# Optimization experiments

Measured on AMD Instinct MI355X. Metric: run time of the kernel, lower is better.

## Reference

```python
import jax, jax.numpy as jnp
import numpy as np

BETA = 0.25
STRIDE = 64  # LCCombine: ConvTranspose1d with ones kernel, kernel_size == stride


def setup_inputs() -> dict:
    key = jax.random.key(0)
    k0, k1, k2, k3 = jax.random.split(key, 4)
    B, Q, K, N = 2, 64, 512, 1024
    n_classes = 256
    n_wav = N * STRIDE - 1
    quant_pred = jax.random.normal(k0, (B, n_classes, n_wav), dtype=jnp.float32)
    ze = jax.random.normal(k1, (B, Q, N), dtype=jnp.float32)
    emb = jax.random.normal(k2, (K, N), dtype=jnp.float32)
    target_wav = jax.random.randint(k3, (B, 1, n_wav), 0, n_classes)
    return {"quant_pred": quant_pred, "ze": ze, "emb": emb, "target_wav": target_wav}


def _combine(x):
    # LCCombine: replicate each bottleneck-rate value over STRIDE wav steps
    # (transposed conv, ones kernel, kernel==stride), then drop last step.
    # x: (B, N) -> (B, 1, N*STRIDE - 1)
    return jnp.repeat(x, STRIDE, axis=-1)[:, None, :-1]


def reference(quant_pred, ze, emb, target_wav):
    # l2 loss: stop-grad on ze (codebook update term)
    sg_ze = jax.lax.stop_gradient(ze)
    d = sg_ze[:, :, None, :] - emb[None, None, :, :]      # (B, Q, K, N)
    l2_loss = jnp.min(jnp.sum(d * d, axis=1), axis=1)      # (B, N)
    # commitment loss: stop-grad on emb
    sg_emb = jax.lax.stop_gradient(emb)
    dc = ze[:, :, None, :] - sg_emb[None, None, :, :]      # (B, Q, K, N)
    com_loss = jnp.min(jnp.sum(dc * dc, axis=1), axis=1) * BETA  # (B, N)

    l2_loss_comb = _combine(l2_loss)                       # (B, 1, N_wav)
    com_loss_comb = _combine(com_loss)                     # (B, 1, N_wav)

    log_pred = jax.nn.log_softmax(quant_pred, axis=1)      # (B, C, N_wav)
    log_pred_target = jnp.take_along_axis(log_pred, target_wav, axis=1)  # (B,1,N_wav)

    total_loss_terms = log_pred_target + l2_loss_comb + com_loss_comb
    return jnp.mean(total_loss_terms)
```

## Files before the change

### kernel.cpp

```cpp
#include <hip/hip_runtime.h>


#define QQ   64
#define NN   1024
#define KK   512
#define CLS  256
#define NW   65535

__global__ __launch_bounds__(64) void vq_l2min_kernel(
        const float* __restrict__ ze,
        const float* __restrict__ emb,
        float* __restrict__ l2ws,
        float* __restrict__ out) {
    int bn = blockIdx.x;
    int b  = bn >> 10;
    int n  = bn & (NN - 1);
    int lane = threadIdx.x;

    float v  = ze[(size_t)(b * QQ + lane) * NN + n];
    float s1 = v, s2 = v * v;
    #pragma unroll
    for (int m = 32; m >= 1; m >>= 1) {
        s1 += __shfl_xor(s1, m, 64);
        s2 += __shfl_xor(s2, m, 64);
    }

    float best = 3.4e38f;
    float n2s1 = -2.0f * s1;
    #pragma unroll
    for (int j = 0; j < KK / 64; ++j) {
        float e = emb[(size_t)(lane + 64 * j) * NN + n];
        float c = fmaf(e, fmaf((float)QQ, e, n2s1), s2);
        best = fminf(best, c);
    }
    #pragma unroll
    for (int m = 32; m >= 1; m >>= 1)
        best = fminf(best, __shfl_xor(best, m, 64));

    if (lane == 0) l2ws[bn] = 1.25f * best;
    if (bn == 0 && lane == 0) out[0] = 0.0f;
}

__global__ __launch_bounds__(256) void vq_lse_kernel(
        const float* __restrict__ qp,
        const int*   __restrict__ tgt,
        const float* __restrict__ l2ws,
        float* __restrict__ out) {
    int g = blockIdx.x * 256 + threadIdx.x;
    int b = g >> 16;
    int t = g & 0xFFFF;

    float contrib = 0.0f;
    if (t < NW) {
        const float* p = qp + (size_t)b * CLS * NW + t;
        int   tg = tgt[(size_t)b * NW + t];
        float m = -3.4e38f, s = 0.0f, tv = 0.0f;
        #pragma unroll 4
        for (int c = 0; c < CLS; c += 4) {
            float x0 = p[(size_t)(c + 0) * NW];
            float x1 = p[(size_t)(c + 1) * NW];
            float x2 = p[(size_t)(c + 2) * NW];
            float x3 = p[(size_t)(c + 3) * NW];
            if (tg == c + 0) tv = x0;
            if (tg == c + 1) tv = x1;
            if (tg == c + 2) tv = x2;
            if (tg == c + 3) tv = x3;
            float m01 = fmaxf(x0, x1), m23 = fmaxf(x2, x3);
            float m4  = fmaxf(m01, m23);
            float s4  = __expf(x0 - m4) + __expf(x1 - m4)
                      + __expf(x2 - m4) + __expf(x3 - m4);
            float nm  = fmaxf(m, m4);
            s = s * __expf(m - nm) + s4 * __expf(m4 - nm);
            m = nm;
        }
        float lse = m + __logf(s);
        contrib = tv - lse + l2ws[b * NN + (t >> 6)];
    }

    #pragma unroll
    for (int msk = 32; msk >= 1; msk >>= 1)
        contrib += __shfl_xor(contrib, msk, 64);

    __shared__ float part[4];
    int lane = threadIdx.x & 63, wv = threadIdx.x >> 6;
    if (lane == 0) part[wv] = contrib;
    __syncthreads();
    if (threadIdx.x == 0) {
        float blk = part[0] + part[1] + part[2] + part[3];
        atomicAdd(out, blk * (1.0f / 131070.0f));
    }
}

extern "C" void kernel_launch(void* const* d_in, const int* in_sizes, int n_in,
                              void* d_out, int out_size, void* d_ws, size_t ws_size,
                              hipStream_t stream) {
    const float* quant_pred = (const float*)d_in[0];
    const float* ze         = (const float*)d_in[1];
    const float* emb        = (const float*)d_in[2];
    const int*   target     = (const int*)  d_in[3];
    float* out  = (float*)d_out;
    float* l2ws = (float*)d_ws;

    vq_l2min_kernel<<<2 * NN, 64, 0, stream>>>(ze, emb, l2ws, out);
    vq_lse_kernel<<<512, 256, 0, stream>>>(quant_pred, target, l2ws, out);
}
```

Before: 202.4 us.

## Fuse VQ min-distance into log-softmax kernel with software-pipelined class loads

After: 203.5 us. Within noise of the previous version (+0.5%).

```diff
diff --git a/kernel.cpp b/kernel.cpp
--- a/kernel.cpp
+++ b/kernel.cpp
@@ -7,82 +7,84 @@
 #define CLS  256
 #define NW   65535
 
-__global__ __launch_bounds__(64) void vq_l2min_kernel(
+__global__ __launch_bounds__(256) void vq_fused_kernel(
+        const float* __restrict__ qp,
         const float* __restrict__ ze,
         const float* __restrict__ emb,
-        float* __restrict__ l2ws,
-        float* __restrict__ out) {
-    int bn = blockIdx.x;
-    int b  = bn >> 10;
-    int n  = bn & (NN - 1);
-    int lane = threadIdx.x;
+        const int*   __restrict__ tgt,
+        float* __restrict__ out)
+{
+    const int g     = blockIdx.x * 256 + threadIdx.x;
+    const int b     = g >> 16;
+    const int t     = g & 0xFFFF;
+    const bool valid = (t < NW);
+    const int tc    = valid ? t : (NW - 1);
+    const int n     = tc >> 6;
+    const int lane  = threadIdx.x & 63;
+
+    const float* p = qp + (size_t)b * CLS * NW + tc;
+
+    int tg = tgt[(size_t)b * NW + tc];
+
+    float cur[8];
+    #pragma unroll
+    for (int u = 0; u < 8; ++u) cur[u] = p[(size_t)u * NW];
 
     float v  = ze[(size_t)(b * QQ + lane) * NN + n];
     float s1 = v, s2 = v * v;
     #pragma unroll
-    for (int m = 32; m >= 1; m >>= 1) {
-        s1 += __shfl_xor(s1, m, 64);
-        s2 += __shfl_xor(s2, m, 64);
+    for (int msk = 32; msk >= 1; msk >>= 1) {
+        s1 += __shfl_xor(s1, msk, 64);
+        s2 += __shfl_xor(s2, msk, 64);
     }
-
     float best = 3.4e38f;
     float n2s1 = -2.0f * s1;
     #pragma unroll
     for (int j = 0; j < KK / 64; ++j) {
         float e = emb[(size_t)(lane + 64 * j) * NN + n];
-        float c = fmaf(e, fmaf((float)QQ, e, n2s1), s2);
-        best = fminf(best, c);
+        float cost = fmaf(e, fmaf((float)QQ, e, n2s1), s2);
+        best = fminf(best, cost);
     }
     #pragma unroll
-    for (int m = 32; m >= 1; m >>= 1)
-        best = fminf(best, __shfl_xor(best, m, 64));
+    for (int msk = 32; msk >= 1; msk >>= 1)
+        best = fminf(best, __shfl_xor(best, msk, 64));
+    const float l2 = 1.25f * best;
 
-    if (lane == 0) l2ws[bn] = 1.25f * best;
-    if (bn == 0 && lane == 0) out[0] = 0.0f;
-}
+    float tv = p[(size_t)tg * NW];
 
-__global__ __launch_bounds__(256) void vq_lse_kernel(
-        const float* __restrict__ qp,
-        const int*   __restrict__ tgt,
-        const float* __restrict__ l2ws,
-        float* __restrict__ out) {
-    int g = blockIdx.x * 256 + threadIdx.x;
-    int b = g >> 16;
-    int t = g & 0xFFFF;
+    float m = -3.4e38f, s = 0.0f;
+    auto merge8 = [&](const float* x) {
+        float m01 = fmaxf(x[0], x[1]), m23 = fmaxf(x[2], x[3]);
+        float m45 = fmaxf(x[4], x[5]), m67 = fmaxf(x[6], x[7]);
+        float m8  = fmaxf(fmaxf(m01, m23), fmaxf(m45, m67));
+        float s8  = __expf(x[0] - m8) + __expf(x[1] - m8)
+                  + __expf(x[2] - m8) + __expf(x[3] - m8)
+                  + __expf(x[4] - m8) + __expf(x[5] - m8)
+                  + __expf(x[6] - m8) + __expf(x[7] - m8);
+        float nm  = fmaxf(m, m8);
+        s = s * __expf(m - nm) + s8 * __expf(m8 - nm);
+        m = nm;
+    };
 
-    float contrib = 0.0f;
-    if (t < NW) {
-        const float* p = qp + (size_t)b * CLS * NW + t;
-        int   tg = tgt[(size_t)b * NW + t];
-        float m = -3.4e38f, s = 0.0f, tv = 0.0f;
-        #pragma unroll 4
-        for (int c = 0; c < CLS; c += 4) {
-            float x0 = p[(size_t)(c + 0) * NW];
-            float x1 = p[(size_t)(c + 1) * NW];
-            float x2 = p[(size_t)(c + 2) * NW];
-            float x3 = p[(size_t)(c + 3) * NW];
-            if (tg == c + 0) tv = x0;
-            if (tg == c + 1) tv = x1;
-            if (tg == c + 2) tv = x2;
-            if (tg == c + 3) tv = x3;
-            float m01 = fmaxf(x0, x1), m23 = fmaxf(x2, x3);
-            float m4  = fmaxf(m01, m23);
-            float s4  = __expf(x0 - m4) + __expf(x1 - m4)
-                      + __expf(x2 - m4) + __expf(x3 - m4);
-            float nm  = fmaxf(m, m4);
-            s = s * __expf(m - nm) + s4 * __expf(m4 - nm);
-            m = nm;
-        }
-        float lse = m + __logf(s);
-        contrib = tv - lse + l2ws[b * NN + (t >> 6)];
+    for (int c = 8; c < CLS; c += 8) {
+        float nxt[8];
+        #pragma unroll
+        for (int u = 0; u < 8; ++u) nxt[u] = p[(size_t)(c + u) * NW];
+        merge8(cur);
+        #pragma unroll
+        for (int u = 0; u < 8; ++u) cur[u] = nxt[u];
     }
+    merge8(cur);
+
+    float lse = m + __logf(s);
+    float contrib = valid ? (tv - lse + l2) : 0.0f;
 
     #pragma unroll
     for (int msk = 32; msk >= 1; msk >>= 1)
         contrib += __shfl_xor(contrib, msk, 64);
 
     __shared__ float part[4];
-    int lane = threadIdx.x & 63, wv = threadIdx.x >> 6;
+    int wv = threadIdx.x >> 6;
     if (lane == 0) part[wv] = contrib;
     __syncthreads();
     if (threadIdx.x == 0) {
@@ -98,9 +100,9 @@
     const float* ze         = (const float*)d_in[1];
     const float* emb        = (const float*)d_in[2];
     const int*   target     = (const int*)  d_in[3];
-    float* out  = (float*)d_out;
-    float* l2ws = (float*)d_ws;
+    float* out = (float*)d_out;
+    (void)d_ws; (void)ws_size; (void)in_sizes; (void)n_in; (void)out_size;
 
-    vq_l2min_kernel<<<2 * NN, 64, 0, stream>>>(ze, emb, l2ws, out);
-    vq_lse_kernel<<<512, 256, 0, stream>>>(quant_pred, target, l2ws, out);
+    hipMemsetAsync(out, 0, sizeof(float), stream);
+    vq_fused_kernel<<<512, 256, 0, stream>>>(quant_pred, ze, emb, target, out);
 }
```
